# Kernel tuning notes

Measured on AMD Instinct MI355X. Metric: run time of the kernel, lower is better.

Reference implementation:

```python
import jax, jax.numpy as jnp
import numpy as np

B, T, D, H = 4, 2048, 1024, 16
HD = D // H

def setup_inputs() -> dict:
    key = jax.random.key(0)
    ks = jax.random.split(key, 5)
    s = 0.02
    return {
        "x": jax.random.normal(ks[0], (B, T, D), dtype=jnp.float32),
        "w_qkv": jax.random.normal(ks[1], (D, 3 * D), dtype=jnp.float32) * s,
        "b_qkv": jax.random.normal(ks[2], (3 * D,), dtype=jnp.float32) * s,
        "w_proj": jax.random.normal(ks[3], (D, D), dtype=jnp.float32) * s,
        "b_proj": jax.random.normal(ks[4], (D,), dtype=jnp.float32) * s,
    }

def reference(x, w_qkv, b_qkv, w_proj, b_proj):
    b, t, c = x.shape
    h, hd = H, HD
    scale = hd ** -0.5
    qkv = x @ w_qkv + b_qkv                       # [B,T,3D]
    qkv = qkv.reshape(b, t, 3, h, hd)
    q, k, v = qkv[:, :, 0], qkv[:, :, 1], qkv[:, :, 2]   # [B,T,H,HD]
    # scores [B,H,T,T]
    att = jnp.einsum('bqhd,bkhd->bhqk', q, k) * scale
    causal = jnp.tril(jnp.ones((t, t), dtype=bool))
    att = jnp.where(causal[None, None], att, -jnp.inf)
    w = jax.nn.softmax(att, axis=-1)
    out = jnp.einsum('bhqk,bkhd->bqhd', w, v).reshape(b, t, c)
    return out @ w_proj + b_proj
```

## Files before the change

### kernel.cpp

```cpp
#include <hip/hip_runtime.h>
#include <hip/hip_bf16.h>
#include <cstdint>

#define BB 4
#define TT 2048
#define DD 1024
#define HH 16
#define HD 64
#define MM (BB*TT)
#define NQKV (3*DD)
#define QSCALE 0.18033688f
#define NQT 16

typedef __bf16 bf16;
typedef __bf16 bf16x8 __attribute__((ext_vector_type(8)));
typedef float f32x4 __attribute__((ext_vector_type(4)));

#define AS1 __attribute__((address_space(1)))
#define AS3 __attribute__((address_space(3)))

__device__ __forceinline__ void gload_lds16(const void* g, void* l) {
  __builtin_amdgcn_global_load_lds((const AS1 uint32_t*)g, (AS3 uint32_t*)l, 16, 0, 0);
}

__global__ void k_cvt_x(const float* __restrict__ in, bf16* __restrict__ out) {
  int i = blockIdx.x * blockDim.x + threadIdx.x;
  float4 v = ((const float4*)in)[i];
  ushort4 o;
  o.x = __builtin_bit_cast(unsigned short, (bf16)v.x);
  o.y = __builtin_bit_cast(unsigned short, (bf16)v.y);
  o.z = __builtin_bit_cast(unsigned short, (bf16)v.z);
  o.w = __builtin_bit_cast(unsigned short, (bf16)v.w);
  ((ushort4*)out)[i] = o;
}

__global__ void k_transpose_w(const float* __restrict__ in, bf16* __restrict__ out,
                              int R, int C) {
  __shared__ float tile[32][33];
  const int c0 = blockIdx.x * 32, r0 = blockIdx.y * 32;
  const int tx = threadIdx.x & 31, ty = threadIdx.x >> 5;
#pragma unroll
  for (int i = 0; i < 32; i += 8)
    tile[ty + i][tx] = in[(long)(r0 + ty + i) * C + c0 + tx];
  __syncthreads();
#pragma unroll
  for (int i = 0; i < 32; i += 8)
    out[(long)(c0 + ty + i) * R + r0 + tx] = (bf16)tile[tx][ty + i];
}

template <int EPI>
__global__ __launch_bounds__(256) void k_gemm(
    const bf16* __restrict__ A, const bf16* __restrict__ Bt,
    const float* __restrict__ bias, float* __restrict__ fout,
    bf16* __restrict__ q_out, bf16* __restrict__ k_out, bf16* __restrict__ v_out,
    int K) {
  __shared__ bf16 sm[2 * 128 * 64];
  bf16* const As = sm;
  bf16* const Bs = sm + 128 * 64;
  const int tid = threadIdx.x;
  const int m0 = blockIdx.x * 128;
  const int n0 = blockIdx.y * 128;
  const int wv = tid >> 6, lane = tid & 63;
  const int g = lane >> 4, lr = lane & 15;
  const int wm = (wv >> 1) * 64, wn = (wv & 1) * 64;
  const int sr = tid >> 3, sc = tid & 7;
  f32x4 acc[4][4] = {};

  for (int k0 = 0; k0 < K; k0 += 64) {
#pragma unroll
    for (int p = 0; p < 4; ++p) {
      const int row = p * 32 + sr;
      const int chunk = sc ^ (row & 7);
      gload_lds16(A + ((long)(m0 + row) * K + k0 + (chunk << 3)),
                  As + (row << 6) + (sc << 3));
      gload_lds16(Bt + ((long)(n0 + row) * K + k0 + (chunk << 3)),
                  Bs + (row << 6) + (sc << 3));
    }
    __syncthreads();
#pragma unroll
    for (int kf = 0; kf < 2; ++kf) {
      bf16x8 af[4], bfr[4];
#pragma unroll
      for (int mf = 0; mf < 4; ++mf) {
        const int row = wm + mf * 16 + lr;
        af[mf] = *(const bf16x8*)((const char*)As +
                 (((row << 7) + (kf << 6) + (g << 4)) ^ ((row & 7) << 4)));
      }
#pragma unroll
      for (int nf = 0; nf < 4; ++nf) {
        const int row = wn + nf * 16 + lr;
        bfr[nf] = *(const bf16x8*)((const char*)Bs +
                 (((row << 7) + (kf << 6) + (g << 4)) ^ ((row & 7) << 4)));
      }
#pragma unroll
      for (int mf = 0; mf < 4; ++mf)
#pragma unroll
        for (int nf = 0; nf < 4; ++nf)
          acc[mf][nf] = __builtin_amdgcn_mfma_f32_16x16x32_bf16(af[mf], bfr[nf],
                                                                acc[mf][nf], 0, 0, 0);
    }
    __syncthreads();
  }

  if (EPI == 0) {
    const int sel = n0 >> 10;
    const int d0 = n0 & 1023;
    const int b = m0 >> 11;
    const int t0 = m0 & 2047;
    const int h0 = d0 >> 6;
    if (sel < 2) {
      const float qs = (sel == 0) ? QSCALE : 1.0f;
      bf16* Cs = sm;
#pragma unroll
      for (int nf = 0; nf < 4; ++nf) {
        const int col = wn + nf * 16 + lr;
        const float bv = bias[n0 + col];
#pragma unroll
        for (int mf = 0; mf < 4; ++mf)
#pragma unroll
          for (int j = 0; j < 4; ++j) {
            const int row = wm + mf * 16 + g * 4 + j;
            const float v = (acc[mf][nf][j] + bv) * qs;
            const int cp = (col >> 3) ^ (((row >> 2) & 3) << 1);
            Cs[(row << 7) + (cp << 3) + (col & 7)] = (bf16)v;
          }
      }
      __syncthreads();
      bf16* dst = (sel == 0) ? q_out : k_out;
#pragma unroll
      for (int i = 0; i < 8; ++i) {
        const int cid = (i << 8) + tid;
        const int hh = cid >> 10;
        const int r  = (cid >> 3) & 127;
        const int ck = cid & 7;
        const int cp = ((hh << 3) + ck) ^ (((r >> 2) & 3) << 1);
        const bf16x8 vv = *(const bf16x8*)&Cs[(r << 7) + (cp << 3)];
        const long off = ((((long)b * HH + h0 + hh) * TT + t0 + r) << 6) + (ck << 3);
        *(bf16x8*)(dst + off) = vv;
      }
    } else {
      bf16* Cs = sm;
#pragma unroll
      for (int nf = 0; nf < 4; ++nf) {
        const int col = wn + nf * 16 + lr;
        const float bv = bias[n0 + col];
#pragma unroll
        for (int mf = 0; mf < 4; ++mf) {
          const int row0 = wm + mf * 16 + g * 4;
          ushort4 pk;
          pk.x = __builtin_bit_cast(unsigned short, (bf16)(acc[mf][nf][0] + bv));
          pk.y = __builtin_bit_cast(unsigned short, (bf16)(acc[mf][nf][1] + bv));
          pk.z = __builtin_bit_cast(unsigned short, (bf16)(acc[mf][nf][2] + bv));
          pk.w = __builtin_bit_cast(unsigned short, (bf16)(acc[mf][nf][3] + bv));
          *(ushort4*)((char*)Cs + ((col << 8) + ((row0 << 1) ^ ((col & 7) << 4)))) = pk;
        }
      }
      __syncthreads();
#pragma unroll
      for (int i = 0; i < 8; ++i) {
        const int cid = (i << 8) + tid;
        const int c  = cid >> 4;
        const int ck = cid & 15;
        const bf16x8 vv = *(const bf16x8*)((const char*)Cs +
                           ((c << 8) + ((ck << 4) ^ ((c & 7) << 4))));
        const int hh = c >> 6, hd = c & 63;
        const long off = (((long)b * HH + h0 + hh) * HD + hd) * TT + t0 + (ck << 3);
        *(bf16x8*)(v_out + off) = vv;
      }
    }
  } else {
    float* Cf = (float*)sm;
#pragma unroll
    for (int pass = 0; pass < 2; ++pass) {
      __syncthreads();
      if ((wm >> 6) == pass) {
#pragma unroll
        for (int nf = 0; nf < 4; ++nf) {
          const int col = wn + nf * 16 + lr;
          const float bv = bias[n0 + col];
#pragma unroll
          for (int mf = 0; mf < 4; ++mf)
#pragma unroll
            for (int j = 0; j < 4; ++j) {
              const int row = mf * 16 + g * 4 + j;
              const int cp = (col >> 2) ^ (((row >> 2) & 3) << 1);
              Cf[(row << 7) + (cp << 2) + (col & 3)] = acc[mf][nf][j] + bv;
            }
        }
      }
      __syncthreads();
#pragma unroll
      for (int i = 0; i < 8; ++i) {
        const int cid = (i << 8) + tid;
        const int r  = cid >> 5;
        const int ck = cid & 31;
        const int cp = ck ^ (((r >> 2) & 3) << 1);
        const float4 vv = *(const float4*)&Cf[(r << 7) + (cp << 2)];
        const long rowm = m0 + (pass << 6) + r;
        *(float4*)&fout[rowm * DD + n0 + (ck << 2)] = vv;
      }
    }
  }
}

template <bool MASKED>
__device__ __forceinline__ void attn_tile(
    const bf16* __restrict__ Kt, const bf16* __restrict__ Vt,
    bf16* __restrict__ Pw, const bf16x8 (&qf)[2][2],
    f32x4 (&acc)[2][4], f32x4 (&ls)[2],
    int rowbase, int kv0, int g, int lr, bf16x8 ones) {
  f32x4 s[2][4] = {};
#pragma unroll
  for (int kf = 0; kf < 2; ++kf) {
    bf16x8 bfr[4];
#pragma unroll
    for (int nf = 0; nf < 4; ++nf) {
      const int row = nf * 16 + lr;
      bfr[nf] = *(const bf16x8*)((const char*)Kt +
               (((row << 7) + (kf << 6) + (g << 4)) ^ ((row & 7) << 4)));
    }
#pragma unroll
    for (int mf = 0; mf < 2; ++mf)
#pragma unroll
      for (int nf = 0; nf < 4; ++nf)
        s[mf][nf] = __builtin_amdgcn_mfma_f32_16x16x32_bf16(qf[mf][kf], bfr[nf],
                                                            s[mf][nf], 0, 0, 0);
  }
#pragma unroll
  for (int mf = 0; mf < 2; ++mf) {
#pragma unroll
    for (int nf = 0; nf < 4; ++nf) {
      const int col = kv0 + nf * 16 + lr;
#pragma unroll
      for (int j = 0; j < 4; ++j) {
        float p;
        if (MASKED) {
          const int rowq = rowbase + mf * 16 + g * 4 + j;
          p = (col <= rowq) ? __builtin_amdgcn_exp2f(s[mf][nf][j]) : 0.f;
        } else {
          p = __builtin_amdgcn_exp2f(s[mf][nf][j]);
        }
        const int prow = mf * 16 + g * 4 + j;
        const int pcol = nf * 16 + lr;
        *(bf16*)((char*)Pw +
                 (((prow << 7) + (pcol << 1)) ^ ((prow & 7) << 4))) = (bf16)p;
      }
    }
  }
#pragma unroll
  for (int kf = 0; kf < 2; ++kf) {
    bf16x8 pa[2], vb[4];
#pragma unroll
    for (int mf = 0; mf < 2; ++mf) {
      const int row = mf * 16 + lr;
      pa[mf] = *(const bf16x8*)((const char*)Pw +
               (((row << 7) + (kf << 6) + (g << 4)) ^ ((row & 7) << 4)));
    }
#pragma unroll
    for (int nf = 0; nf < 4; ++nf) {
      const int row = nf * 16 + lr;
      vb[nf] = *(const bf16x8*)((const char*)Vt +
               (((row << 7) + (kf << 6) + (g << 4)) ^ ((row & 7) << 4)));
    }
#pragma unroll
    for (int mf = 0; mf < 2; ++mf)
      ls[mf] = __builtin_amdgcn_mfma_f32_16x16x32_bf16(pa[mf], ones, ls[mf], 0, 0, 0);
#pragma unroll
    for (int mf = 0; mf < 2; ++mf)
#pragma unroll
      for (int nf = 0; nf < 4; ++nf)
        acc[mf][nf] = __builtin_amdgcn_mfma_f32_16x16x32_bf16(pa[mf], vb[nf],
                                                              acc[mf][nf], 0, 0, 0);
  }
}

__global__ __launch_bounds__(256, 2) void k_attn(
    const bf16* __restrict__ Q, const bf16* __restrict__ K,
    const bf16* __restrict__ Vt, bf16* __restrict__ O) {
  __shared__ bf16 Ks[2][64 * 64];
  __shared__ bf16 Vs[2][64 * 64];
  __shared__ bf16 Ps[4][32 * 64];
  const int tid = threadIdx.x;
  const int qa = blockIdx.x, qb = NQT - 1 - qa;
  const int bh = blockIdx.y;
  const int b = bh >> 4, h = bh & 15;
  const int wv = tid >> 6, lane = tid & 63;
  const int g = lane >> 4, lr = lane & 15;
  const int ra = qa * 128 + wv * 32;
  const int rb = qb * 128 + wv * 32;
  const bf16* Qb = Q + (long)bh * TT * HD;
  const bf16* Kb = K + (long)bh * TT * HD;
  const bf16* Vb = Vt + (long)bh * HD * TT;
  bf16* Pw = &Ps[wv][0];

  bf16x8 ones;
#pragma unroll
  for (int i = 0; i < 8; ++i) ones[i] = (bf16)1.0f;

  bf16x8 qfa[2][2], qfb[2][2];
#pragma unroll
  for (int mf = 0; mf < 2; ++mf)
#pragma unroll
    for (int kf = 0; kf < 2; ++kf) {
      qfa[mf][kf] = *(const bf16x8*)(Qb + ((long)(ra + mf * 16 + lr) << 6) +
                                     kf * 32 + g * 8);
      qfb[mf][kf] = *(const bf16x8*)(Qb + ((long)(rb + mf * 16 + lr) << 6) +
                                     kf * 32 + g * 8);
    }

  f32x4 acca[2][4] = {}, accb[2][4] = {};
  f32x4 lsa[2] = {}, lsb[2] = {};

  const int sr = tid >> 3, sc = tid & 7;
  const int nkv = 2 * qb + 2;

  auto STAGE = [&](int buf, int kt) {
    const int kv0 = kt * 64;
#pragma unroll
    for (int p = 0; p < 2; ++p) {
      const int row = p * 32 + sr;
      const int chunk = sc ^ (row & 7);
      gload_lds16(Kb + ((long)(kv0 + row) << 6) + (chunk << 3),
                  &Ks[buf][(row << 6) + (sc << 3)]);
      gload_lds16(Vb + (long)row * TT + kv0 + (chunk << 3),
                  &Vs[buf][(row << 6) + (sc << 3)]);
    }
  };

  STAGE(0, 0);
  __syncthreads();

  int cur = 0;
  for (int kt = 0; kt < nkv; ++kt) {
    const int kv0 = kt * 64;
    if (kt + 1 < nkv) STAGE(cur ^ 1, kt + 1);

    const bf16* Kt  = &Ks[cur][0];
    const bf16* Vtl = &Vs[cur][0];
    if (kv0 + 63 <= ra)
      attn_tile<false>(Kt, Vtl, Pw, qfa, acca, lsa, ra, kv0, g, lr, ones);
    else if (kv0 <= ra + 31)
      attn_tile<true >(Kt, Vtl, Pw, qfa, acca, lsa, ra, kv0, g, lr, ones);
    if (kv0 + 63 <= rb)
      attn_tile<false>(Kt, Vtl, Pw, qfb, accb, lsb, rb, kv0, g, lr, ones);
    else if (kv0 <= rb + 31)
      attn_tile<true >(Kt, Vtl, Pw, qfb, accb, lsb, rb, kv0, g, lr, ones);

    __syncthreads();
    cur ^= 1;
  }

#pragma unroll
  for (int mf = 0; mf < 2; ++mf) {
    float inva[4], invb[4];
#pragma unroll
    for (int j = 0; j < 4; ++j) {
      inva[j] = 1.0f / lsa[mf][j];
      invb[j] = 1.0f / lsb[mf][j];
    }
#pragma unroll
    for (int nf = 0; nf < 4; ++nf) {
      const int col = h * 64 + nf * 16 + lr;
#pragma unroll
      for (int j = 0; j < 4; ++j) {
        const int ta = ra + mf * 16 + g * 4 + j;
        const int tb = rb + mf * 16 + g * 4 + j;
        O[(((long)b * TT + ta) << 10) + col] = (bf16)(acca[mf][nf][j] * inva[j]);
        O[(((long)b * TT + tb) << 10) + col] = (bf16)(accb[mf][nf][j] * invb[j]);
      }
    }
  }
}

extern "C" void kernel_launch(void* const* d_in, const int* in_sizes, int n_in,
                              void* d_out, int out_size, void* d_ws, size_t ws_size,
                              hipStream_t stream) {
  (void)in_sizes; (void)n_in; (void)out_size; (void)ws_size;
  const float* x      = (const float*)d_in[0];
  const float* w_qkv  = (const float*)d_in[1];
  const float* b_qkv  = (const float*)d_in[2];
  const float* w_proj = (const float*)d_in[3];
  const float* b_proj = (const float*)d_in[4];
  float* out = (float*)d_out;

  bf16* ws = (bf16*)d_ws;
  const long NX = (long)MM * DD;
  bf16* xb     = ws;
  bf16* wqkvT  = xb + NX;
  bf16* wprojT = wqkvT + (long)NQKV * DD;
  bf16* Qb     = wprojT + (long)DD * DD;
  bf16* Kb     = Qb + NX;
  bf16* Vtb    = Kb + NX;
  bf16* attout = xb;

  k_cvt_x<<<(int)(NX / 4 / 256), 256, 0, stream>>>(x, xb);
  k_transpose_w<<<dim3(NQKV / 32, DD / 32), 256, 0, stream>>>(w_qkv, wqkvT, DD, NQKV);
  k_transpose_w<<<dim3(DD / 32, DD / 32), 256, 0, stream>>>(w_proj, wprojT, DD, DD);
  k_gemm<0><<<dim3(MM / 128, NQKV / 128), 256, 0, stream>>>(
      xb, wqkvT, b_qkv, nullptr, Qb, Kb, Vtb, DD);
  k_attn<<<dim3(NQT / 2, BB * HH), 256, 0, stream>>>(Qb, Kb, Vtb, attout);
  k_gemm<1><<<dim3(MM / 128, DD / 128), 256, 0, stream>>>(
      attout, wprojT, b_proj, out, nullptr, nullptr, nullptr, DD);
}
```

Measured before the change: 174.4 us.

## Merge prep kernels and split attention into one query tile per block

The x conversion and the two weight transposes are folded into a single k_prep launch that picks its work by block index, saving two kernel launches. The attention kernel no longer pairs a low and a high query tile per block. Each block now handles one 128-row query tile, with heaviest tiles launched first, so the grid doubles to 1024 blocks and occupancy is raised to 3 blocks per CU. The trade-off is that each K/V tile staged into LDS is now reused by only one query tile instead of two, which increases K/V global traffic and leaves the load balance to the hardware scheduler.

```diff
diff --git a/kernel.cpp b/kernel.cpp
--- a/kernel.cpp
+++ b/kernel.cpp
@@ -23,21 +23,32 @@
   __builtin_amdgcn_global_load_lds((const AS1 uint32_t*)g, (AS3 uint32_t*)l, 16, 0, 0);
 }
 
-__global__ void k_cvt_x(const float* __restrict__ in, bf16* __restrict__ out) {
-  int i = blockIdx.x * blockDim.x + threadIdx.x;
-  float4 v = ((const float4*)in)[i];
-  ushort4 o;
-  o.x = __builtin_bit_cast(unsigned short, (bf16)v.x);
-  o.y = __builtin_bit_cast(unsigned short, (bf16)v.y);
-  o.z = __builtin_bit_cast(unsigned short, (bf16)v.z);
-  o.w = __builtin_bit_cast(unsigned short, (bf16)v.w);
-  ((ushort4*)out)[i] = o;
-}
-
-__global__ void k_transpose_w(const float* __restrict__ in, bf16* __restrict__ out,
-                              int R, int C) {
+__global__ void k_prep(const float* __restrict__ x, bf16* __restrict__ xb,
+                       const float* __restrict__ wqkv, bf16* __restrict__ wqkvT,
+                       const float* __restrict__ wproj, bf16* __restrict__ wprojT) {
   __shared__ float tile[32][33];
-  const int c0 = blockIdx.x * 32, r0 = blockIdx.y * 32;
+  const int bid = blockIdx.x;
+  if (bid < 8192) {
+    const int i = bid * 256 + threadIdx.x;
+    float4 v = ((const float4*)x)[i];
+    ushort4 o;
+    o.x = __builtin_bit_cast(unsigned short, (bf16)v.x);
+    o.y = __builtin_bit_cast(unsigned short, (bf16)v.y);
+    o.z = __builtin_bit_cast(unsigned short, (bf16)v.z);
+    o.w = __builtin_bit_cast(unsigned short, (bf16)v.w);
+    ((ushort4*)xb)[i] = o;
+    return;
+  }
+  const float* in; bf16* out; int R, C, c0, r0;
+  if (bid < 8192 + 3072) {
+    const int id = bid - 8192;
+    in = wqkv; out = wqkvT; R = DD; C = NQKV;
+    c0 = (id % 96) * 32; r0 = (id / 96) * 32;
+  } else {
+    const int id = bid - 8192 - 3072;
+    in = wproj; out = wprojT; R = DD; C = DD;
+    c0 = (id % 32) * 32; r0 = (id / 32) * 32;
+  }
   const int tx = threadIdx.x & 31, ty = threadIdx.x >> 5;
 #pragma unroll
   for (int i = 0; i < 32; i += 8)
@@ -274,20 +285,19 @@
   }
 }
 
-__global__ __launch_bounds__(256, 2) void k_attn(
+__global__ __launch_bounds__(256, 3) void k_attn(
     const bf16* __restrict__ Q, const bf16* __restrict__ K,
     const bf16* __restrict__ Vt, bf16* __restrict__ O) {
   __shared__ bf16 Ks[2][64 * 64];
   __shared__ bf16 Vs[2][64 * 64];
   __shared__ bf16 Ps[4][32 * 64];
   const int tid = threadIdx.x;
-  const int qa = blockIdx.x, qb = NQT - 1 - qa;
+  const int qa = NQT - 1 - blockIdx.x;
   const int bh = blockIdx.y;
   const int b = bh >> 4, h = bh & 15;
   const int wv = tid >> 6, lane = tid & 63;
   const int g = lane >> 4, lr = lane & 15;
   const int ra = qa * 128 + wv * 32;
-  const int rb = qb * 128 + wv * 32;
   const bf16* Qb = Q + (long)bh * TT * HD;
   const bf16* Kb = K + (long)bh * TT * HD;
   const bf16* Vb = Vt + (long)bh * HD * TT;
@@ -297,22 +307,19 @@
 #pragma unroll
   for (int i = 0; i < 8; ++i) ones[i] = (bf16)1.0f;
 
-  bf16x8 qfa[2][2], qfb[2][2];
+  bf16x8 qfa[2][2];
 #pragma unroll
   for (int mf = 0; mf < 2; ++mf)
 #pragma unroll
-    for (int kf = 0; kf < 2; ++kf) {
+    for (int kf = 0; kf < 2; ++kf)
       qfa[mf][kf] = *(const bf16x8*)(Qb + ((long)(ra + mf * 16 + lr) << 6) +
                                      kf * 32 + g * 8);
-      qfb[mf][kf] = *(const bf16x8*)(Qb + ((long)(rb + mf * 16 + lr) << 6) +
-                                     kf * 32 + g * 8);
-    }
-
-  f32x4 acca[2][4] = {}, accb[2][4] = {};
-  f32x4 lsa[2] = {}, lsb[2] = {};
+
+  f32x4 acca[2][4] = {};
+  f32x4 lsa[2] = {};
 
   const int sr = tid >> 3, sc = tid & 7;
-  const int nkv = 2 * qb + 2;
+  const int nkv = 2 * qa + 2;
 
   auto STAGE = [&](int buf, int kt) {
     const int kv0 = kt * 64;
@@ -341,10 +348,6 @@
       attn_tile<false>(Kt, Vtl, Pw, qfa, acca, lsa, ra, kv0, g, lr, ones);
     else if (kv0 <= ra + 31)
       attn_tile<true >(Kt, Vtl, Pw, qfa, acca, lsa, ra, kv0, g, lr, ones);
-    if (kv0 + 63 <= rb)
-      attn_tile<false>(Kt, Vtl, Pw, qfb, accb, lsb, rb, kv0, g, lr, ones);
-    else if (kv0 <= rb + 31)
-      attn_tile<true >(Kt, Vtl, Pw, qfb, accb, lsb, rb, kv0, g, lr, ones);
 
     __syncthreads();
     cur ^= 1;
@@ -352,21 +355,16 @@
 
 #pragma unroll
   for (int mf = 0; mf < 2; ++mf) {
-    float inva[4], invb[4];
-#pragma unroll
-    for (int j = 0; j < 4; ++j) {
-      inva[j] = 1.0f / lsa[mf][j];
-      invb[j] = 1.0f / lsb[mf][j];
-    }
+    float inva[4];
+#pragma unroll
+    for (int j = 0; j < 4; ++j) inva[j] = 1.0f / lsa[mf][j];
 #pragma unroll
     for (int nf = 0; nf < 4; ++nf) {
       const int col = h * 64 + nf * 16 + lr;
 #pragma unroll
       for (int j = 0; j < 4; ++j) {
         const int ta = ra + mf * 16 + g * 4 + j;
-        const int tb = rb + mf * 16 + g * 4 + j;
         O[(((long)b * TT + ta) << 10) + col] = (bf16)(acca[mf][nf][j] * inva[j]);
-        O[(((long)b * TT + tb) << 10) + col] = (bf16)(accb[mf][nf][j] * invb[j]);
       }
     }
   }
@@ -393,12 +391,10 @@
   bf16* Vtb    = Kb + NX;
   bf16* attout = xb;
 
-  k_cvt_x<<<(int)(NX / 4 / 256), 256, 0, stream>>>(x, xb);
-  k_transpose_w<<<dim3(NQKV / 32, DD / 32), 256, 0, stream>>>(w_qkv, wqkvT, DD, NQKV);
-  k_transpose_w<<<dim3(DD / 32, DD / 32), 256, 0, stream>>>(w_proj, wprojT, DD, DD);
+  k_prep<<<8192 + 3072 + 1024, 256, 0, stream>>>(x, xb, w_qkv, wqkvT, w_proj, wprojT);
   k_gemm<0><<<dim3(MM / 128, NQKV / 128), 256, 0, stream>>>(
       xb, wqkvT, b_qkv, nullptr, Qb, Kb, Vtb, DD);
-  k_attn<<<dim3(NQT / 2, BB * HH), 256, 0, stream>>>(Qb, Kb, Vtb, attout);
+  k_attn<<<dim3(NQT, BB * HH), 256, 0, stream>>>(Qb, Kb, Vtb, attout);
   k_gemm<1><<<dim3(MM / 128, DD / 128), 256, 0, stream>>>(
       attout, wprojT, b_proj, out, nullptr, nullptr, nullptr, DD);
 }
```

Result: slower. 232.8 us (+33.5%).
